# Kernel optimization log

Measured on AMD Instinct MI355X. Metric: run time of the kernel, lower is better.

## Reference

```python
import jax, jax.numpy as jnp
import numpy as np

B, C, H, W = 32, 384, 28, 28
E, HID, K = 4, 384, 2  # HID = hidden_features(1536) // num_experts(4)


def setup_inputs() -> dict:
    key = jax.random.key(0)
    ks = jax.random.split(key, 5)
    x = jax.random.normal(ks[0], (B, C, H, W), jnp.float32)
    gate_w = jax.random.normal(ks[1], (C, E), jnp.float32) * 0.02
    gate_b = jnp.zeros((E,), jnp.float32)
    w1 = jax.random.normal(ks[2], (E, HID, C), jnp.float32) * 0.02
    b1 = jnp.zeros((E, HID), jnp.float32)
    w2 = jax.random.normal(ks[3], (E, C, HID), jnp.float32) * 0.02
    b2 = jnp.zeros((E, C), jnp.float32)
    return {"x": x, "gate_w": gate_w, "gate_b": gate_b,
            "w1": w1, "b1": b1, "w2": w2, "b2": b2}


def reference(x, gate_w, gate_b, w1, b1, w2, b2):
    b, c, h, w = x.shape
    e = gate_b.shape[0]
    # per-token gating: tokens are spatial positions in NHWC order
    x_flat = x.transpose(0, 2, 3, 1).reshape(-1, c)          # [N, C], N = B*H*W
    scores = jax.nn.softmax(x_flat @ gate_w + gate_b, -1)    # [N, E]
    top_v, top_i = jax.lax.top_k(scores, K)                  # [N, K]
    top_w = jax.nn.softmax(top_v, -1)                        # [N, K] renormalized
    # weight map per top-k slot: [K, B, H, W]
    wmap = top_w.T.reshape(K, b, h, w)
    # faithful to torch loop: expert i contributes at slot k iff ANY token routed
    # to it at slot k; the weight applied is the UNMASKED slot-k weight map.
    present = (top_i[:, :, None] == jnp.arange(e)[None, None, :]).any(0)  # [K, E]
    coef = jnp.einsum('ke,kbhw->ebhw', present.astype(x.dtype), wmap)     # [E, B, H, W]
    # dense per-expert 1x1-conv MLP over the FULL tensor (as in the source)
    hdn = jax.nn.relu(jnp.einsum('bchw,edc->ebdhw', x, w1)
                      + b1[:, None, :, None, None])          # [E, B, HID, H, W]
    y = jnp.einsum('ebdhw,eod->ebohw', hdn, w2) + b2[:, None, :, None, None]
    out = jnp.einsum('ebohw,ebhw->bohw', y, coef)            # [B, C, H, W]
    return out
```

## Files before the change

kernel.cpp:

```cpp
#include <hip/hip_runtime.h>
#include <hip/hip_bf16.h>
#include <stdint.h>

#define B_DIM 32
#define C_DIM 384
#define HW_DIM 784
#define E_DIM 4
#define HID_DIM 384
#define NTOK (B_DIM * HW_DIM)
#define NH (E_DIM * HID_DIM)

using short8 = __attribute__((ext_vector_type(8))) short;
using f32x4  = __attribute__((ext_vector_type(4))) float;
typedef unsigned short ushort_t;

__device__ __forceinline__ ushort_t f2bf(float f) {
  __hip_bfloat16 h = __float2bfloat16(f);
  return __builtin_bit_cast(ushort_t, h);
}

__device__ __forceinline__ void gload_lds16(const void* g, void* l) {
  __builtin_amdgcn_global_load_lds(
      (const __attribute__((address_space(1))) unsigned int*)g,
      (__attribute__((address_space(3))) unsigned int*)l, 16, 0, 0);
}

__global__ __launch_bounds__(256) void prep_kernel(
    const float* __restrict__ w1, const float* __restrict__ w2,
    ushort_t* __restrict__ W1b, ushort_t* __restrict__ W2b,
    unsigned int* __restrict__ present) {
  int i = blockIdx.x * 256 + threadIdx.x;
  if (i == 0) *present = 0u;
  if (i < NH * C_DIM) {
    W1b[i] = f2bf(w1[i]);
    int o = i / NH;
    int r = i - o * NH;
    int e = r / HID_DIM;
    int k = r - e * HID_DIM;
    W2b[i] = f2bf(w2[((size_t)e * C_DIM + o) * HID_DIM + k]);
  }
}

__global__ __launch_bounds__(512) void gate_kernel(
    const float* __restrict__ x, const float* __restrict__ gw,
    const float* __restrict__ gb, ushort_t* __restrict__ xb,
    float* __restrict__ topw, unsigned int* __restrict__ present) {
  __shared__ __align__(16) ushort_t lxs[64][392];
  __shared__ float pscore[8][64][4];
  __shared__ unsigned int pmask;
  const int b = blockIdx.x;
  const int p0 = blockIdx.y * 64;
  const int cnt = min(64, HW_DIM - p0);
  const int tid = threadIdx.x;
  const int cg = tid >> 6, tl = tid & 63;
  if (tid == 0) pmask = 0u;
  float a0 = 0.f, a1 = 0.f, a2 = 0.f, a3 = 0.f;
  const bool valid = tl < cnt;
  if (valid) {
    const float* xp = x + (size_t)b * C_DIM * HW_DIM + p0 + tl;
    for (int c = cg; c < C_DIM; c += 8) {
      const float v = xp[(size_t)c * HW_DIM];
      lxs[tl][c] = f2bf(v);
      const float4 g = *(const float4*)&gw[c * 4];
      a0 += v * g.x; a1 += v * g.y; a2 += v * g.z; a3 += v * g.w;
    }
  }
  pscore[cg][tl][0] = a0; pscore[cg][tl][1] = a1;
  pscore[cg][tl][2] = a2; pscore[cg][tl][3] = a3;
  __syncthreads();
  if (cg == 0 && valid) {
    float z[4];
#pragma unroll
    for (int e = 0; e < 4; e++) {
      float s = gb[e];
#pragma unroll
      for (int g8 = 0; g8 < 8; g8++) s += pscore[g8][tl][e];
      z[e] = s;
    }
    const float mx = fmaxf(fmaxf(z[0], z[1]), fmaxf(z[2], z[3]));
    float s[4]; float sum = 0.f;
#pragma unroll
    for (int e = 0; e < 4; e++) { s[e] = __expf(z[e] - mx); sum += s[e]; }
    const float inv = 1.f / sum;
#pragma unroll
    for (int e = 0; e < 4; e++) s[e] *= inv;
    int e0 = 0; float v0 = s[0];
#pragma unroll
    for (int e = 1; e < 4; e++) if (s[e] > v0) { v0 = s[e]; e0 = e; }
    int e1 = -1; float v1 = -1.f;
#pragma unroll
    for (int e = 0; e < 4; e++) if (e != e0 && s[e] > v1) { v1 = s[e]; e1 = e; }
    const float r = __expf(v1 - v0);
    const float w0 = 1.f / (1.f + r);
    const int m = b * HW_DIM + p0 + tl;
    topw[m * 2] = w0;
    topw[m * 2 + 1] = 1.f - w0;
    atomicOr(&pmask, (1u << e0) | (1u << (4 + e1)));
  }
  __syncthreads();
  if (tid == 0) atomicOr(present, pmask);
  const int nchunk = cnt * 48;
  for (int ci = tid; ci < nchunk; ci += 512) {
    const int row = ci / 48, c8 = ci - row * 48;
    short8 v = *(const short8*)&lxs[row][c8 * 8];
    *(short8*)&xb[(size_t)(b * HW_DIM + p0 + row) * C_DIM + c8 * 8] = v;
  }
}

__global__ __launch_bounds__(128, 2) void gemm_w2(
    const ushort_t* __restrict__ A, const ushort_t* __restrict__ Bw,
    const float* __restrict__ bias, const float* __restrict__ topw,
    const unsigned int* __restrict__ presentp, ushort_t* __restrict__ hOut) {
  constexpr int KDIM = C_DIM, BM = 128, BN = 128, BK = 32;
  constexpr int KT = KDIM / BK;
  constexpr int NTN = NH / BN;
  constexpr int ASZ = BM * BK;
  __shared__ ushort_t smem[4 * ASZ];

  const int nwg = NTN * (NTOK / BM);
  const int orig = blockIdx.x;
  const int xcd = orig & 7;
  const int qq = nwg >> 3, rr = nwg & 7;
  const int wg = (xcd < rr ? xcd * (qq + 1) : rr * (qq + 1) + (xcd - rr) * qq)
               + (orig >> 3);
  const int mt = wg / NTN, nt = wg % NTN;
  const int m0 = mt * BM, n0 = nt * BN;

  const int tid = threadIdx.x;
  const int lane = tid & 63;
  const int wn = tid >> 6;
  const int lanel = lane & 15, laneq = lane >> 4;

  auto stage = [&](int t) {
    ushort_t* dstA = smem + (t & 1) * ASZ;
    ushort_t* dstB = smem + 2 * ASZ + (t & 1) * ASZ;
    const int kb = t * BK;
#pragma unroll
    for (int li = 0; li < 4; ++li) {
      const int P = (li * 128 + tid) * 16;
      const int row = P >> 6;
      const int cb = (P & 63) ^ (((row >> 1) & 3) << 4);
      gload_lds16(&A[(size_t)(m0 + row) * KDIM + kb + (cb >> 1)],
                  (char*)dstA + P);
    }
#pragma unroll
    for (int li = 0; li < 4; ++li) {
      const int P = (li * 128 + tid) * 16;
      const int row = P >> 6;
      const int cb = (P & 63) ^ (((row >> 1) & 3) << 4);
      gload_lds16(&Bw[(size_t)(n0 + row) * KDIM + kb + (cb >> 1)],
                  (char*)dstB + P);
    }
  };

  f32x4 acc[8][4] = {};
  const int cbr = (laneq * 16) ^ (((lanel >> 1) & 3) << 4);

  stage(0);
  for (int t = 0; t < KT; ++t) {
    asm volatile("s_waitcnt vmcnt(0)" ::: "memory");
    __builtin_amdgcn_sched_barrier(0);
    __builtin_amdgcn_s_barrier();
    __builtin_amdgcn_sched_barrier(0);
    if (t + 1 < KT) stage(t + 1);
    const char* Ab = (const char*)(smem + (t & 1) * ASZ) + lanel * 64;
    const char* Bb = (const char*)(smem + 2 * ASZ + (t & 1) * ASZ) +
                     (wn * 64 + lanel) * 64;
    short8 av[8], bv[4];
#pragma unroll
    for (int i = 0; i < 8; ++i) av[i] = *(const short8*)(Ab + i * 1024 + cbr);
#pragma unroll
    for (int j = 0; j < 4; ++j) bv[j] = *(const short8*)(Bb + j * 1024 + cbr);
    __builtin_amdgcn_s_setprio(1);
#pragma unroll
    for (int i = 0; i < 8; ++i)
#pragma unroll
      for (int j = 0; j < 4; ++j)
        acc[i][j] = __builtin_amdgcn_mfma_f32_16x16x32_bf16(
            av[i], bv[j], acc[i][j], 0, 0, 0);
    __builtin_amdgcn_s_setprio(0);
  }

  const unsigned int pm = *presentp;
  __syncthreads();
  ushort_t* tr = smem;
  const int e = n0 / HID_DIM;
  const float P0 = (float)((pm >> e) & 1u);
  const float P1 = (float)((pm >> (4 + e)) & 1u);
#pragma unroll
  for (int mi = 0; mi < 8; ++mi) {
    const int r0 = mi * 16 + laneq * 4;
    const int mg = m0 + r0;
    const float4 t0 = *(const float4*)&topw[mg * 2];
    const float4 t1 = *(const float4*)&topw[mg * 2 + 4];
    const float cj[4] = {P0 * t0.x + P1 * t0.y, P0 * t0.z + P1 * t0.w,
                         P0 * t1.x + P1 * t1.y, P0 * t1.z + P1 * t1.w};
#pragma unroll
    for (int ni = 0; ni < 4; ++ni) {
      const int cl = wn * 64 + ni * 16 + lanel;
      const float bvv = bias[n0 + cl];
#pragma unroll
      for (int j = 0; j < 4; ++j) {
        float v = fmaxf(acc[mi][ni][j] + bvv, 0.f);
        tr[(r0 + j) * 128 + cl] = f2bf(cj[j] * v);
      }
    }
  }
  __syncthreads();
#pragma unroll
  for (int it = 0; it < 16; ++it) {
    const int c = it * 128 + tid;
    const int row = c >> 4, cr = c & 15;
    *(short8*)&hOut[(size_t)(m0 + row) * NH + n0 + cr * 8] =
        *(const short8*)&tr[row * 128 + cr * 8];
  }
}

__global__ __launch_bounds__(256, 3) void gemm2_k(
    const ushort_t* __restrict__ A, const ushort_t* __restrict__ Bw,
    const float* __restrict__ bias, const float* __restrict__ topw,
    const unsigned int* __restrict__ presentp, float* __restrict__ outp) {
  constexpr int KDIM = NH, BM = 128, BN = 128, BK = 32;
  constexpr int KT = KDIM / BK;
  constexpr int NTN = C_DIM / BN;
  constexpr int ASZ = BM * BK;
  __shared__ ushort_t smem[6 * ASZ];

  const int nwg = NTN * (NTOK / BM);
  const int orig = blockIdx.x;
  const int xcd = orig & 7;
  const int qq = nwg >> 3, rr = nwg & 7;
  const int wg = (xcd < rr ? xcd * (qq + 1) : rr * (qq + 1) + (xcd - rr) * qq)
               + (orig >> 3);
  const int mt = wg / NTN, nt = wg % NTN;
  const int m0 = mt * BM, n0 = nt * BN;

  const int tid = threadIdx.x;
  const int lane = tid & 63;
  const int wid = tid >> 6;
  const int wm = wid >> 1, wn = wid & 1;
  const int lanel = lane & 15, laneq = lane >> 4;

  auto stage = [&](int t) {
    const int buf = t % 3;
    ushort_t* dstA = smem + buf * ASZ;
    ushort_t* dstB = smem + 3 * ASZ + buf * ASZ;
    const int kb = t * BK;
#pragma unroll
    for (int li = 0; li < 2; ++li) {
      const int P = (li * 256 + tid) * 16;
      const int row = P >> 6;
      const int cb = (P & 63) ^ (((row >> 1) & 3) << 4);
      gload_lds16(&A[(size_t)(m0 + row) * KDIM + kb + (cb >> 1)],
                  (char*)dstA + P);
    }
#pragma unroll
    for (int li = 0; li < 2; ++li) {
      const int P = (li * 256 + tid) * 16;
      const int row = P >> 6;
      const int cb = (P & 63) ^ (((row >> 1) & 3) << 4);
      gload_lds16(&Bw[(size_t)(n0 + row) * KDIM + kb + (cb >> 1)],
                  (char*)dstB + P);
    }
  };

  f32x4 acc[4][4] = {};
  const int cbr = (laneq * 16) ^ (((lanel >> 1) & 3) << 4);

  stage(0);
  stage(1);
  for (int t = 0; t < KT; ++t) {
    if (t + 1 < KT)
      asm volatile("s_waitcnt vmcnt(4)" ::: "memory");
    else
      asm volatile("s_waitcnt vmcnt(0)" ::: "memory");
    __builtin_amdgcn_sched_barrier(0);
    __builtin_amdgcn_s_barrier();
    __builtin_amdgcn_sched_barrier(0);
    if (t + 2 < KT) stage(t + 2);
    const int buf = t % 3;
    const char* Ab = (const char*)(smem + buf * ASZ) + (wm * 64 + lanel) * 64;
    const char* Bb =
        (const char*)(smem + 3 * ASZ + buf * ASZ) + (wn * 64 + lanel) * 64;
    short8 av[4], bv[4];
#pragma unroll
    for (int i = 0; i < 4; ++i) av[i] = *(const short8*)(Ab + i * 1024 + cbr);
#pragma unroll
    for (int j = 0; j < 4; ++j) bv[j] = *(const short8*)(Bb + j * 1024 + cbr);
    __builtin_amdgcn_s_setprio(1);
#pragma unroll
    for (int i = 0; i < 4; ++i)
#pragma unroll
      for (int j = 0; j < 4; ++j)
        acc[i][j] = __builtin_amdgcn_mfma_f32_16x16x32_bf16(
            av[i], bv[j], acc[i][j], 0, 0, 0);
    __builtin_amdgcn_s_setprio(0);
  }

  const unsigned int pm = *presentp;
  float B0[4], B1[4];
#pragma unroll
  for (int ni = 0; ni < 4; ++ni) {
    const int o = n0 + wn * 64 + ni * 16 + lanel;
    float s0 = 0.f, s1 = 0.f;
#pragma unroll
    for (int e2 = 0; e2 < 4; ++e2) {
      const float bb = bias[e2 * C_DIM + o];
      s0 += (float)((pm >> e2) & 1u) * bb;
      s1 += (float)((pm >> (4 + e2)) & 1u) * bb;
    }
    B0[ni] = s0; B1[ni] = s1;
  }
#pragma unroll
  for (int mi = 0; mi < 4; ++mi) {
    const int mg = m0 + wm * 64 + mi * 16 + laneq * 4;
    const float4 t0 = *(const float4*)&topw[mg * 2];
    const float4 t1 = *(const float4*)&topw[mg * 2 + 4];
    const int bb2 = mg / HW_DIM;
    const int p = mg - bb2 * HW_DIM;
#pragma unroll
    for (int ni = 0; ni < 4; ++ni) {
      const int o = n0 + wn * 64 + ni * 16 + lanel;
      float4 v;
      v.x = acc[mi][ni][0] + t0.x * B0[ni] + t0.y * B1[ni];
      v.y = acc[mi][ni][1] + t0.z * B0[ni] + t0.w * B1[ni];
      v.z = acc[mi][ni][2] + t1.x * B0[ni] + t1.y * B1[ni];
      v.w = acc[mi][ni][3] + t1.z * B0[ni] + t1.w * B1[ni];
      *(float4*)&outp[((size_t)bb2 * C_DIM + o) * HW_DIM + p] = v;
    }
  }
}

extern "C" void kernel_launch(void* const* d_in, const int* in_sizes, int n_in,
                              void* d_out, int out_size, void* d_ws, size_t ws_size,
                              hipStream_t stream) {
  const float* x  = (const float*)d_in[0];
  const float* gw = (const float*)d_in[1];
  const float* gb = (const float*)d_in[2];
  const float* w1 = (const float*)d_in[3];
  const float* b1 = (const float*)d_in[4];
  const float* w2 = (const float*)d_in[5];
  const float* b2 = (const float*)d_in[6];
  float* out = (float*)d_out;

  char* ws = (char*)d_ws;
  ushort_t* xb = (ushort_t*)ws;   ws += (size_t)NTOK * C_DIM * 2;
  ushort_t* hdnS = (ushort_t*)ws; ws += (size_t)NTOK * NH * 2;
  ushort_t* W1b = (ushort_t*)ws;  ws += (size_t)NH * C_DIM * 2;
  ushort_t* W2b = (ushort_t*)ws;  ws += (size_t)C_DIM * NH * 2;
  float* topw = (float*)ws;       ws += (size_t)NTOK * 2 * 4;
  unsigned int* present = (unsigned int*)ws;

  prep_kernel<<<dim3((NH * C_DIM) / 256), dim3(256), 0, stream>>>(
      w1, w2, W1b, W2b, present);
  gate_kernel<<<dim3(B_DIM, 13), dim3(512), 0, stream>>>(
      x, gw, gb, xb, topw, present);
  gemm_w2<<<dim3((NTOK / 128) * (NH / 128)), dim3(128), 0, stream>>>(
      xb, W1b, b1, topw, present, hdnS);
  gemm2_k<<<dim3((NTOK / 128) * (C_DIM / 128)), dim3(256), 0, stream>>>(
      hdnS, W2b, b2, topw, present, out);
}
```

Baseline: 128.7 us.

## Swap GEMM kernel configs and pre-swizzle W2 into MFMA fragment layout

The first GEMM now uses the 4-wave, 3-stage-pipelined kernel body that previously ran the second GEMM, with the ReLU/gate epilogue moved into it. The second GEMM becomes a 2-wave kernel that reads W2 straight from global memory into registers. The prep kernel rewrites W2 into a pre-swizzled per-lane fragment layout so these loads are coalesced and skip LDS, and A gets a 3-buffer LDS ring with two tiles in flight. This is meant to cut LDS traffic and barrier stalls for the weight operand. The cost is more registers and reliance on hand-tuned vmcnt counts.

After: 116.7 us (median of 2 runs). -9.4%, faster.

```diff
diff --git a/kernel.cpp b/kernel.cpp
--- a/kernel.cpp
+++ b/kernel.cpp
@@ -9,6 +9,7 @@
 #define HID_DIM 384
 #define NTOK (B_DIM * HW_DIM)
 #define NH (E_DIM * HID_DIM)
+#define WSZ 589824
 
 using short8 = __attribute__((ext_vector_type(8))) short;
 using f32x4  = __attribute__((ext_vector_type(4))) float;
@@ -27,17 +28,24 @@
 
 __global__ __launch_bounds__(256) void prep_kernel(
     const float* __restrict__ w1, const float* __restrict__ w2,
-    ushort_t* __restrict__ W1b, ushort_t* __restrict__ W2b,
+    ushort_t* __restrict__ W1b, ushort_t* __restrict__ W2f,
     unsigned int* __restrict__ present) {
   int i = blockIdx.x * 256 + threadIdx.x;
   if (i == 0) *present = 0u;
-  if (i < NH * C_DIM) {
-    W1b[i] = f2bf(w1[i]);
-    int o = i / NH;
-    int r = i - o * NH;
-    int e = r / HID_DIM;
-    int k = r - e * HID_DIM;
-    W2b[i] = f2bf(w2[((size_t)e * C_DIM + o) * HID_DIM + k]);
+  if (i >= WSZ) return;
+  W1b[i] = f2bf(w1[i]);
+  {
+    int r = i;
+    const int nt = r / 196608; r -= nt * 196608;
+    const int ks = r / 4096;   r -= ks * 4096;
+    const int wn = r >> 11;
+    const int ni = (r >> 9) & 3;
+    const int ln = (r >> 3) & 63;
+    const int tt = r & 7;
+    const int o = nt * 128 + wn * 64 + ni * 16 + (ln & 15);
+    const int kg = ks * 32 + (ln >> 4) * 8 + tt;
+    const int e = kg / HID_DIM, d = kg - e * HID_DIM;
+    W2f[i] = f2bf(w2[((size_t)e * C_DIM + o) * HID_DIM + d]);
   }
 }
 
@@ -107,122 +115,13 @@
   }
 }
 
-__global__ __launch_bounds__(128, 2) void gemm_w2(
+__global__ __launch_bounds__(256, 3) void gemm_1b(
     const ushort_t* __restrict__ A, const ushort_t* __restrict__ Bw,
     const float* __restrict__ bias, const float* __restrict__ topw,
     const unsigned int* __restrict__ presentp, ushort_t* __restrict__ hOut) {
   constexpr int KDIM = C_DIM, BM = 128, BN = 128, BK = 32;
   constexpr int KT = KDIM / BK;
   constexpr int NTN = NH / BN;
-  constexpr int ASZ = BM * BK;
-  __shared__ ushort_t smem[4 * ASZ];
-
-  const int nwg = NTN * (NTOK / BM);
-  const int orig = blockIdx.x;
-  const int xcd = orig & 7;
-  const int qq = nwg >> 3, rr = nwg & 7;
-  const int wg = (xcd < rr ? xcd * (qq + 1) : rr * (qq + 1) + (xcd - rr) * qq)
-               + (orig >> 3);
-  const int mt = wg / NTN, nt = wg % NTN;
-  const int m0 = mt * BM, n0 = nt * BN;
-
-  const int tid = threadIdx.x;
-  const int lane = tid & 63;
-  const int wn = tid >> 6;
-  const int lanel = lane & 15, laneq = lane >> 4;
-
-  auto stage = [&](int t) {
-    ushort_t* dstA = smem + (t & 1) * ASZ;
-    ushort_t* dstB = smem + 2 * ASZ + (t & 1) * ASZ;
-    const int kb = t * BK;
-#pragma unroll
-    for (int li = 0; li < 4; ++li) {
-      const int P = (li * 128 + tid) * 16;
-      const int row = P >> 6;
-      const int cb = (P & 63) ^ (((row >> 1) & 3) << 4);
-      gload_lds16(&A[(size_t)(m0 + row) * KDIM + kb + (cb >> 1)],
-                  (char*)dstA + P);
-    }
-#pragma unroll
-    for (int li = 0; li < 4; ++li) {
-      const int P = (li * 128 + tid) * 16;
-      const int row = P >> 6;
-      const int cb = (P & 63) ^ (((row >> 1) & 3) << 4);
-      gload_lds16(&Bw[(size_t)(n0 + row) * KDIM + kb + (cb >> 1)],
-                  (char*)dstB + P);
-    }
-  };
-
-  f32x4 acc[8][4] = {};
-  const int cbr = (laneq * 16) ^ (((lanel >> 1) & 3) << 4);
-
-  stage(0);
-  for (int t = 0; t < KT; ++t) {
-    asm volatile("s_waitcnt vmcnt(0)" ::: "memory");
-    __builtin_amdgcn_sched_barrier(0);
-    __builtin_amdgcn_s_barrier();
-    __builtin_amdgcn_sched_barrier(0);
-    if (t + 1 < KT) stage(t + 1);
-    const char* Ab = (const char*)(smem + (t & 1) * ASZ) + lanel * 64;
-    const char* Bb = (const char*)(smem + 2 * ASZ + (t & 1) * ASZ) +
-                     (wn * 64 + lanel) * 64;
-    short8 av[8], bv[4];
-#pragma unroll
-    for (int i = 0; i < 8; ++i) av[i] = *(const short8*)(Ab + i * 1024 + cbr);
-#pragma unroll
-    for (int j = 0; j < 4; ++j) bv[j] = *(const short8*)(Bb + j * 1024 + cbr);
-    __builtin_amdgcn_s_setprio(1);
-#pragma unroll
-    for (int i = 0; i < 8; ++i)
-#pragma unroll
-      for (int j = 0; j < 4; ++j)
-        acc[i][j] = __builtin_amdgcn_mfma_f32_16x16x32_bf16(
-            av[i], bv[j], acc[i][j], 0, 0, 0);
-    __builtin_amdgcn_s_setprio(0);
-  }
-
-  const unsigned int pm = *presentp;
-  __syncthreads();
-  ushort_t* tr = smem;
-  const int e = n0 / HID_DIM;
-  const float P0 = (float)((pm >> e) & 1u);
-  const float P1 = (float)((pm >> (4 + e)) & 1u);
-#pragma unroll
-  for (int mi = 0; mi < 8; ++mi) {
-    const int r0 = mi * 16 + laneq * 4;
-    const int mg = m0 + r0;
-    const float4 t0 = *(const float4*)&topw[mg * 2];
-    const float4 t1 = *(const float4*)&topw[mg * 2 + 4];
-    const float cj[4] = {P0 * t0.x + P1 * t0.y, P0 * t0.z + P1 * t0.w,
-                         P0 * t1.x + P1 * t1.y, P0 * t1.z + P1 * t1.w};
-#pragma unroll
-    for (int ni = 0; ni < 4; ++ni) {
-      const int cl = wn * 64 + ni * 16 + lanel;
-      const float bvv = bias[n0 + cl];
-#pragma unroll
-      for (int j = 0; j < 4; ++j) {
-        float v = fmaxf(acc[mi][ni][j] + bvv, 0.f);
-        tr[(r0 + j) * 128 + cl] = f2bf(cj[j] * v);
-      }
-    }
-  }
-  __syncthreads();
-#pragma unroll
-  for (int it = 0; it < 16; ++it) {
-    const int c = it * 128 + tid;
-    const int row = c >> 4, cr = c & 15;
-    *(short8*)&hOut[(size_t)(m0 + row) * NH + n0 + cr * 8] =
-        *(const short8*)&tr[row * 128 + cr * 8];
-  }
-}
-
-__global__ __launch_bounds__(256, 3) void gemm2_k(
-    const ushort_t* __restrict__ A, const ushort_t* __restrict__ Bw,
-    const float* __restrict__ bias, const float* __restrict__ topw,
-    const unsigned int* __restrict__ presentp, float* __restrict__ outp) {
-  constexpr int KDIM = NH, BM = 128, BN = 128, BK = 32;
-  constexpr int KT = KDIM / BK;
-  constexpr int NTN = C_DIM / BN;
   constexpr int ASZ = BM * BK;
   __shared__ ushort_t smem[6 * ASZ];
 
@@ -298,6 +197,123 @@
   }
 
   const unsigned int pm = *presentp;
+  __syncthreads();
+  ushort_t* tr = smem;
+  const int e = n0 / HID_DIM;
+  const float P0 = (float)((pm >> e) & 1u);
+  const float P1 = (float)((pm >> (4 + e)) & 1u);
+#pragma unroll
+  for (int mi = 0; mi < 4; ++mi) {
+    const int r0 = wm * 64 + mi * 16 + laneq * 4;
+    const int mg = m0 + r0;
+    const float4 t0 = *(const float4*)&topw[mg * 2];
+    const float4 t1 = *(const float4*)&topw[mg * 2 + 4];
+    const float cj[4] = {P0 * t0.x + P1 * t0.y, P0 * t0.z + P1 * t0.w,
+                         P0 * t1.x + P1 * t1.y, P0 * t1.z + P1 * t1.w};
+#pragma unroll
+    for (int ni = 0; ni < 4; ++ni) {
+      const int cl = wn * 64 + ni * 16 + lanel;
+      const float bvv = bias[n0 + cl];
+#pragma unroll
+      for (int j = 0; j < 4; ++j) {
+        float v = fmaxf(acc[mi][ni][j] + bvv, 0.f);
+        tr[(r0 + j) * 128 + cl] = f2bf(cj[j] * v);
+      }
+    }
+  }
+  __syncthreads();
+#pragma unroll
+  for (int it = 0; it < 8; ++it) {
+    const int c = it * 256 + tid;
+    const int row = c >> 4, cr = c & 15;
+    *(short8*)&hOut[(size_t)(m0 + row) * NH + n0 + cr * 8] =
+        *(const short8*)&tr[row * 128 + cr * 8];
+  }
+}
+
+__global__ __launch_bounds__(128, 2) void gemm_bd(
+    const ushort_t* __restrict__ A, const ushort_t* __restrict__ Wf,
+    const float* __restrict__ bias, const float* __restrict__ topw,
+    const unsigned int* __restrict__ presentp, float* __restrict__ outp) {
+  constexpr int KDIM = NH, BM = 128, BN = 128, BK = 32;
+  constexpr int KT = KDIM / BK;
+  constexpr int NTN = C_DIM / BN;
+  constexpr int ASZ = BM * BK;
+  __shared__ ushort_t smem[3 * ASZ];
+
+  const int nwg = NTN * (NTOK / BM);
+  const int orig = blockIdx.x;
+  const int xcd = orig & 7;
+  const int qq = nwg >> 3, rr = nwg & 7;
+  const int wg = (xcd < rr ? xcd * (qq + 1) : rr * (qq + 1) + (xcd - rr) * qq)
+               + (orig >> 3);
+  const int mt = wg / NTN, nt = wg % NTN;
+  const int m0 = mt * BM, n0 = nt * BN;
+
+  const int tid = threadIdx.x;
+  const int lane = tid & 63;
+  const int wn = tid >> 6;
+  const int lanel = lane & 15, laneq = lane >> 4;
+
+  const ushort_t* wbase = Wf + (size_t)nt * KT * 4096 + wn * 2048 + lane * 8;
+
+  auto stage = [&](int t) {
+    ushort_t* dst = smem + (t % 3) * ASZ;
+    const int kb = t * BK;
+#pragma unroll
+    for (int li = 0; li < 4; ++li) {
+      const int P = (li * 128 + tid) * 16;
+      const int row = P >> 6;
+      const int cb = (P & 63) ^ (((row >> 1) & 3) << 4);
+      gload_lds16(&A[(size_t)(m0 + row) * KDIM + kb + (cb >> 1)],
+                  (char*)dst + P);
+    }
+  };
+  auto ldB = [&](int t, short8* bv) {
+    const ushort_t* p = wbase + (size_t)t * 4096;
+#pragma unroll
+    for (int j = 0; j < 4; ++j) bv[j] = *(const short8*)(p + j * 512);
+  };
+
+  f32x4 acc[8][4] = {};
+  const int cbr = (laneq * 16) ^ (((lanel >> 1) & 3) << 4);
+
+  short8 bvA[4], bvB[4];
+
+  auto step = [&](int t, short8* cur) {
+    if (t + 1 < KT)
+      asm volatile("s_waitcnt vmcnt(10)" ::: "memory");
+    else
+      asm volatile("s_waitcnt vmcnt(4)" ::: "memory");
+    __builtin_amdgcn_sched_barrier(0);
+    __builtin_amdgcn_s_barrier();
+    __builtin_amdgcn_sched_barrier(0);
+    if (t + 2 < KT) stage(t + 2);
+    const char* Ab = (const char*)(smem + (t % 3) * ASZ) + lanel * 64;
+    short8 av[8];
+#pragma unroll
+    for (int i = 0; i < 8; ++i) av[i] = *(const short8*)(Ab + i * 1024 + cbr);
+    __builtin_amdgcn_s_setprio(1);
+#pragma unroll
+    for (int i = 0; i < 8; ++i)
+#pragma unroll
+      for (int j = 0; j < 4; ++j)
+        acc[i][j] = __builtin_amdgcn_mfma_f32_16x16x32_bf16(
+            av[i], cur[j], acc[i][j], 0, 0, 0);
+    __builtin_amdgcn_s_setprio(0);
+    if (t + 2 < KT) ldB(t + 2, cur);
+  };
+
+  stage(0);
+  ldB(0, bvA);
+  stage(1);
+  ldB(1, bvB);
+  for (int t = 0; t < KT; t += 2) {
+    step(t, bvA);
+    step(t + 1, bvB);
+  }
+
+  const unsigned int pm = *presentp;
   float B0[4], B1[4];
 #pragma unroll
   for (int ni = 0; ni < 4; ++ni) {
@@ -312,8 +328,8 @@
     B0[ni] = s0; B1[ni] = s1;
   }
 #pragma unroll
-  for (int mi = 0; mi < 4; ++mi) {
-    const int mg = m0 + wm * 64 + mi * 16 + laneq * 4;
+  for (int mi = 0; mi < 8; ++mi) {
+    const int mg = m0 + mi * 16 + laneq * 4;
     const float4 t0 = *(const float4*)&topw[mg * 2];
     const float4 t1 = *(const float4*)&topw[mg * 2 + 4];
     const int bb2 = mg / HW_DIM;
@@ -346,17 +362,17 @@
   char* ws = (char*)d_ws;
   ushort_t* xb = (ushort_t*)ws;   ws += (size_t)NTOK * C_DIM * 2;
   ushort_t* hdnS = (ushort_t*)ws; ws += (size_t)NTOK * NH * 2;
-  ushort_t* W1b = (ushort_t*)ws;  ws += (size_t)NH * C_DIM * 2;
-  ushort_t* W2b = (ushort_t*)ws;  ws += (size_t)C_DIM * NH * 2;
+  ushort_t* W1b = (ushort_t*)ws;  ws += (size_t)WSZ * 2;
+  ushort_t* W2f = (ushort_t*)ws;  ws += (size_t)WSZ * 2;
   float* topw = (float*)ws;       ws += (size_t)NTOK * 2 * 4;
   unsigned int* present = (unsigned int*)ws;
 
-  prep_kernel<<<dim3((NH * C_DIM) / 256), dim3(256), 0, stream>>>(
-      w1, w2, W1b, W2b, present);
+  prep_kernel<<<dim3(WSZ / 256), dim3(256), 0, stream>>>(
+      w1, w2, W1b, W2f, present);
   gate_kernel<<<dim3(B_DIM, 13), dim3(512), 0, stream>>>(
       x, gw, gb, xb, topw, present);
-  gemm_w2<<<dim3((NTOK / 128) * (NH / 128)), dim3(128), 0, stream>>>(
+  gemm_1b<<<dim3((NTOK / 128) * (NH / 128)), dim3(256), 0, stream>>>(
       xb, W1b, b1, topw, present, hdnS);
-  gemm2_k<<<dim3((NTOK / 128) * (C_DIM / 128)), dim3(256), 0, stream>>>(
-      hdnS, W2b, b2, topw, present, out);
-}
+  gemm_bd<<<dim3((NTOK / 128) * (C_DIM / 128)), dim3(128), 0, stream>>>(
+      hdnS, W2f, b2, topw, present, out);
+}
```
